# Kernel optimization log

Hardware: AMD Instinct MI355X
Metric: run time of the kernel (lower is better)

The kernel has to match this reference:

```python
import jax, jax.numpy as jnp
import numpy as np

V, E, H, B, T, S = 32000, 512, 512, 16, 128, 128


def setup_inputs() -> dict:
    key = jax.random.key(0)
    ks = jax.random.split(key, 12)
    sc_e = 1.0 / np.sqrt(E)
    sc_h = 1.0 / np.sqrt(H)
    emb_table = jax.random.normal(ks[0], (V, E), jnp.float32) * 0.02
    emb_table = emb_table.at[0].set(0.0)  # padding_idx=0
    return {
        "text_vec": jax.random.randint(ks[1], (B, T), 0, V),
        "decoder_hidden": jax.random.normal(ks[2], (1, B, H), jnp.float32),
        "encoder_output": jax.random.normal(ks[3], (B, S, H), jnp.float32),
        "attention_mask": jnp.ones((B, S), jnp.bool_),
        "emb_table": emb_table,
        "w_ih": jax.random.uniform(ks[4], (3 * H, E), jnp.float32, -sc_h, sc_h),
        "w_hh": jax.random.uniform(ks[5], (3 * H, H), jnp.float32, -sc_h, sc_h),
        "b_ih": jax.random.uniform(ks[6], (3 * H,), jnp.float32, -sc_h, sc_h),
        "b_hh": jax.random.uniform(ks[7], (3 * H,), jnp.float32, -sc_h, sc_h),
        "lin_out_w": jax.random.uniform(ks[8], (H, 2 * H), jnp.float32, -1.0 / np.sqrt(2 * H), 1.0 / np.sqrt(2 * H)),
        "out_w": jax.random.uniform(ks[9], (V, H), jnp.float32, -sc_h, sc_h),
        "out_b": jax.random.uniform(ks[10], (V,), jnp.float32, -sc_h, sc_h),
    }


def _gru_cell(x, h, w_ih, w_hh, b_ih, b_hh):
    gi = x @ w_ih.T + b_ih  # [B,3H]
    gh = h @ w_hh.T + b_hh  # [B,3H]
    ir, iz, inn = jnp.split(gi, 3, axis=-1)
    hr, hz, hn = jnp.split(gh, 3, axis=-1)
    r = jax.nn.sigmoid(ir + hr)
    z = jax.nn.sigmoid(iz + hz)
    n = jnp.tanh(inn + r * hn)
    return (1.0 - z) * n + z * h


def reference(text_vec, decoder_hidden, encoder_output, attention_mask,
              emb_table, w_ih, w_hh, b_ih, b_hh, lin_out_w, out_w, out_b):
    # embedding with padding_idx=0 -> zero vector
    emb = emb_table[text_vec] * (text_vec != 0)[..., None].astype(emb_table.dtype)  # [B,T,E]
    neg = jnp.asarray(-1e6, emb.dtype)

    def step(h, x_t):
        h_new = _gru_cell(x_t, h, w_ih, w_hh, b_ih, b_hh)  # [B,H]
        scores = jnp.einsum('bh,bsh->bs', h_new, encoder_output)
        scores = jnp.where(attention_mask, scores, neg)
        attn_w = jax.nn.softmax(scores, axis=-1)  # [B,S]
        mix = jnp.einsum('bs,bsh->bh', attn_w, encoder_output)
        combined = jnp.concatenate([h_new, mix], axis=-1)  # [B,2H]
        attended = jnp.tanh(combined @ lin_out_w.T)  # [B,H]
        return h_new, (attended, attn_w)

    h0 = decoder_hidden[0]  # num_layers == 1
    h_final, (attended_seq, attn_w_log) = jax.lax.scan(step, h0, jnp.swapaxes(emb, 0, 1))
    output = jnp.swapaxes(attended_seq, 0, 1)  # [B,T,H]
    scores = output @ out_w.T + out_b  # [B,T,V]
    return scores, h_final[None], attn_w_log
```

## Files before the change

### kernel.cpp

```cpp
#include <hip/hip_runtime.h>
#include <hip/hip_bf16.h>

#define NV 32000
#define NE 512
#define NH 512
#define NB 16
#define NT 128
#define NS 128

typedef __bf16 bf16x8 __attribute__((ext_vector_type(8)));
typedef float f32x4 __attribute__((ext_vector_type(4)));
typedef const __attribute__((address_space(1))) unsigned int gu32;
typedef __attribute__((address_space(3))) unsigned int lu32;

static constexpr size_t HTAG_OFF  = 0;
static constexpr size_t HDONE_OFF = HTAG_OFF + (size_t)2*NB*NH*8;
static constexpr size_t GI_OFF    = HDONE_OFF + 8192;
static constexpr size_t HALL_OFF  = GI_OFF + (size_t)NT*NB*3*NH*4;
static constexpr size_t MIX_OFF   = HALL_OFF + (size_t)(NT+1)*NB*NH*4;
static constexpr size_t ATTB_OFF  = MIX_OFF + (size_t)NB*NT*NH*4;
static constexpr size_t OWB_OFF   = ATTB_OFF + (size_t)NB*NT*NH*2;
static constexpr size_t WS_NEED   = OWB_OFF + (size_t)NV*NH*2;

__global__ __launch_bounds__(256) void k_pg(const int* __restrict__ tv,
                                            const float* __restrict__ emb,
                                            const float* __restrict__ w_ih,
                                            const float* __restrict__ b_ih,
                                            float* __restrict__ gi_all) {
  __shared__ float sbuf[2048];
  const int g = blockIdx.x;
  const int tid = threadIdx.x;
  float (*As)[64] = (float (*)[64])sbuf;
  float (*Bs)[64] = (float (*)[64])(sbuf + 1024);
  const int n0 = (g % 24) * 64;
  const int m0 = (g / 24) * 64;
  float acc[4][4] = {};
  const int rl = tid >> 2;
  const int kq = (tid & 3) * 4;
  const int tvr = tv[m0 + rl];
  const float* arow = emb + (long long)tvr * NE;
  const int tm = tid & 15, tn = tid >> 4;
  for (int k0 = 0; k0 < NE; k0 += 16) {
    __syncthreads();
    float4 av = make_float4(0.f, 0.f, 0.f, 0.f);
    if (tvr != 0) av = *(const float4*)(arow + k0 + kq);
    float4 bv = *(const float4*)(w_ih + (long long)(n0 + rl) * NE + k0 + kq);
    As[kq + 0][rl] = av.x; As[kq + 1][rl] = av.y; As[kq + 2][rl] = av.z; As[kq + 3][rl] = av.w;
    Bs[kq + 0][rl] = bv.x; Bs[kq + 1][rl] = bv.y; Bs[kq + 2][rl] = bv.z; Bs[kq + 3][rl] = bv.w;
    __syncthreads();
#pragma unroll
    for (int kk = 0; kk < 16; ++kk) {
      float4 a = *(const float4*)&As[kk][tm * 4];
      float4 b = *(const float4*)&Bs[kk][tn * 4];
      float ar[4] = {a.x, a.y, a.z, a.w}, br[4] = {b.x, b.y, b.z, b.w};
#pragma unroll
      for (int i = 0; i < 4; ++i)
#pragma unroll
        for (int j = 0; j < 4; ++j) acc[i][j] = fmaf(ar[i], br[j], acc[i][j]);
    }
  }
#pragma unroll
  for (int i = 0; i < 4; ++i) {
    int r = m0 + tm * 4 + i;
    long long gb = (long long)((r & 127) * 16 + (r >> 7)) * (3 * NH);
#pragma unroll
    for (int j = 0; j < 4; ++j) {
      int jg = n0 + tn * 4 + j;
      gi_all[gb + jg] = acc[i][j] + b_ih[jg];
    }
  }
}

__global__ __launch_bounds__(512, 1) void k_mid(const float* __restrict__ w_hh,
                                                const float* __restrict__ gi_all,
                                                const float* __restrict__ b_hh,
                                                const float* __restrict__ dh,
                                                float* __restrict__ h_all,
                                                unsigned long long* __restrict__ htag,
                                                unsigned int* __restrict__ hdone,
                                                float* __restrict__ d_hf,
                                                const float* __restrict__ enc,
                                                const int* __restrict__ mask,
                                                const float* __restrict__ out_w,
                                                __bf16* __restrict__ owb,
                                                float* __restrict__ d_attn,
                                                float* __restrict__ mixb) {
  __shared__ char smem_raw[86016];
  float* smem = (float*)smem_raw;
  const int tid = threadIdx.x;
  const int bid = blockIdx.x;

  if (bid < 128) {
    const int b = bid & 15, sub = bid >> 4;
    const int hl = tid & 63, kc = tid >> 6;
    const int j = sub * 64 + hl;
    float* hbuf = smem;
    float* part = smem + 512;

    float wg[3][64];
#pragma unroll
    for (int g = 0; g < 3; ++g) {
      const float* wp = w_hh + (long long)(g * 512 + j) * NH + kc * 64;
#pragma unroll
      for (int q4 = 0; q4 < 16; ++q4) {
        float4 w4 = *(const float4*)(wp + q4 * 4);
        wg[g][q4 * 4 + 0] = w4.x; wg[g][q4 * 4 + 1] = w4.y;
        wg[g][q4 * 4 + 2] = w4.z; wg[g][q4 * 4 + 3] = w4.w;
      }
    }
    float bhr = 0.f, bhz = 0.f, bhn = 0.f;
    if (tid < 64) {
      bhr = b_hh[sub * 64 + tid];
      bhz = b_hh[512 + sub * 64 + tid];
      bhn = b_hh[1024 + sub * 64 + tid];
    }

    for (int t = 0; t < NT; ++t) {
      float gr = 0.f, gz = 0.f, gn = 0.f;
      if (tid < 64) {
        const float* gi = gi_all + (long long)(t * 16 + b) * 1536;
        gr = gi[sub * 64 + tid];
        gz = gi[512 + sub * 64 + tid];
        gn = gi[1024 + sub * 64 + tid];
      }
      if (t == 0) {
        hbuf[tid] = dh[b * 512 + tid];
      } else {
        unsigned long long* slot = htag + ((long long)(t & 1) * NB + b) * 512 + tid;
        unsigned long long v = __hip_atomic_load(slot, __ATOMIC_RELAXED, __HIP_MEMORY_SCOPE_AGENT);
        int guard = 0;
        while ((unsigned)(v >> 32) != (unsigned)(t + 1) && ++guard < (1 << 22)) {
          v = __hip_atomic_load(slot, __ATOMIC_RELAXED, __HIP_MEMORY_SCOPE_AGENT);
        }
        union { unsigned u; float f; } c; c.u = (unsigned)v;
        hbuf[tid] = c.f;
      }
      __syncthreads();
      float ar = 0.f, az = 0.f, an = 0.f;
#pragma unroll
      for (int q4 = 0; q4 < 4; ++q4) {
        float4 h4[4];
#pragma unroll
        for (int u = 0; u < 4; ++u) h4[u] = *(const float4*)&hbuf[kc * 64 + q4 * 16 + u * 4];
#pragma unroll
        for (int u = 0; u < 4; ++u) {
          const float hh[4] = {h4[u].x, h4[u].y, h4[u].z, h4[u].w};
#pragma unroll
          for (int v = 0; v < 4; ++v) {
            const int q = q4 * 16 + u * 4 + v;
            ar = fmaf(hh[v], wg[0][q], ar);
            az = fmaf(hh[v], wg[1][q], az);
            an = fmaf(hh[v], wg[2][q], an);
          }
        }
      }
      part[(0 * 8 + kc) * 64 + hl] = ar;
      part[(1 * 8 + kc) * 64 + hl] = az;
      part[(2 * 8 + kc) * 64 + hl] = an;
      __syncthreads();
      if (tid < 64) {
        float sr = bhr, sz = bhz, sn = bhn;
#pragma unroll
        for (int c = 0; c < 8; ++c) {
          sr += part[(0 * 8 + c) * 64 + tid];
          sz += part[(1 * 8 + c) * 64 + tid];
          sn += part[(2 * 8 + c) * 64 + tid];
        }
        float r = 1.f / (1.f + expf(-(gr + sr)));
        float z = 1.f / (1.f + expf(-(gz + sz)));
        float n = tanhf(gn + r * sn);
        float hp = hbuf[sub * 64 + tid];
        float hv = (1.f - z) * n + z * hp;
        if (t < NT - 1) {
          union { float f; unsigned u; } c2; c2.f = hv;
          unsigned long long out = ((unsigned long long)(unsigned)(t + 2) << 32) | c2.u;
          __hip_atomic_store(htag + ((long long)((t + 1) & 1) * NB + b) * 512 + sub * 64 + tid, out,
                             __ATOMIC_RELAXED, __HIP_MEMORY_SCOPE_AGENT);
        }
        __hip_atomic_store(&h_all[(long long)((t + 1) * 16 + b) * 512 + sub * 64 + tid], hv,
                           __ATOMIC_RELAXED, __HIP_MEMORY_SCOPE_AGENT);
        if (t == NT - 1) d_hf[b * 512 + sub * 64 + tid] = hv;
      }
      __syncthreads();
      if (tid == 0)
        __hip_atomic_fetch_add(&hdone[t * 16 + b], 1u, __ATOMIC_RELAXED, __HIP_MEMORY_SCOPE_AGENT);
    }
    return;
  }

  const int cid = bid - 128;
  {
    long long n4 = (long long)NV * NH / 4;
    for (long long i = (long long)cid * 512 + tid; i < n4; i += (long long)128 * 512) {
      float4 v = ((const float4*)out_w)[i];
      union { __bf16 b[4]; float2 f2; } u;
      u.b[0] = (__bf16)v.x; u.b[1] = (__bf16)v.y; u.b[2] = (__bf16)v.z; u.b[3] = (__bf16)v.w;
      *((float2*)((__bf16*)owb + 4 * i)) = u.f2;
    }
  }
  float* hb = smem;
  float* red = smem + 512;
  float* wb = smem + 1024;
  float* sred = smem + 1152;
  for (int it = 0; it < 16; ++it) {
    const int u = it * 128 + cid;
    const int t = u >> 4, b = u & 15;
    if (tid == 0) {
      int guard = 0;
      while (__hip_atomic_load(&hdone[u], __ATOMIC_RELAXED, __HIP_MEMORY_SCOPE_AGENT) < 8u &&
             ++guard < (1 << 25)) {
        __builtin_amdgcn_s_sleep(4);
      }
    }
    __syncthreads();
    hb[tid] = __hip_atomic_load(&h_all[(long long)((t + 1) * 16 + b) * 512 + tid],
                                __ATOMIC_RELAXED, __HIP_MEMORY_SCOPE_AGENT);
    __syncthreads();
    {
      const int s = tid & 127, q = tid >> 7;
      const float* erow = enc + (long long)(b * 128 + s) * 512 + q * 128;
      float p = 0.f;
#pragma unroll 8
      for (int k = 0; k < 128; ++k) p = fmaf(hb[q * 128 + k], erow[k], p);
      red[tid] = p;
    }
    __syncthreads();
    float sc = 0.f;
    if (tid < 128) {
      sc = red[tid] + red[tid + 128] + red[tid + 256] + red[tid + 384];
      if (mask[b * 128 + tid] == 0) sc = -1e6f;
      wb[tid] = sc;
    }
    __syncthreads();
    if (tid < 64) {
      float m2 = fmaxf(wb[tid], wb[tid + 64]);
      for (int off = 32; off; off >>= 1) m2 = fmaxf(m2, __shfl_down(m2, off));
      if (tid == 0) sred[0] = m2;
    }
    __syncthreads();
    if (tid < 128) wb[tid] = expf(sc - sred[0]);
    __syncthreads();
    if (tid < 64) {
      float s2 = wb[tid] + wb[tid + 64];
      for (int off = 32; off; off >>= 1) s2 += __shfl_down(s2, off);
      if (tid == 0) sred[1] = s2;
    }
    __syncthreads();
    {
      float inv = 1.f / sred[1];
      if (tid < 128) {
        float w = wb[tid] * inv;
        wb[tid] = w;
        d_attn[(long long)u * 128 + tid] = w;
      }
    }
    __syncthreads();
    {
      float m = 0.f;
#pragma unroll 8
      for (int s2 = 0; s2 < 128; ++s2)
        m = fmaf(wb[s2], enc[(long long)(b * 128 + s2) * 512 + tid], m);
      mixb[(long long)(b * 128 + t) * 512 + tid] = m;
    }
    __syncthreads();
  }
}

__global__ __launch_bounds__(256) void k_att_lin(const float* __restrict__ h_all,
                                                 const float* __restrict__ mix,
                                                 const float* __restrict__ W,
                                                 __bf16* __restrict__ attout) {
  __shared__ float As[16][64];
  __shared__ float Bs[16][64];
  const int tid = threadIdx.x;
  const int n0 = blockIdx.x * 64;
  const int m0 = blockIdx.y * 64;
  float acc[4][4] = {};
  const int rl = tid >> 2;
  const int kq = (tid & 3) * 4;
  const int tm = tid & 15, tn = tid >> 4;
  const int r_a = m0 + rl;
  const int b_a = r_a >> 7, t_a = r_a & 127;
  const float* hrow = h_all + (long long)((t_a + 1) * 16 + b_a) * 512;
  const float* mrow = mix + (long long)r_a * 512;
  for (int k0 = 0; k0 < 1024; k0 += 16) {
    __syncthreads();
    float4 av = (k0 < 512) ? *(const float4*)(hrow + k0 + kq)
                           : *(const float4*)(mrow + (k0 - 512) + kq);
    float4 bv = *(const float4*)(W + (long long)(n0 + rl) * 1024 + k0 + kq);
    As[kq + 0][rl] = av.x; As[kq + 1][rl] = av.y; As[kq + 2][rl] = av.z; As[kq + 3][rl] = av.w;
    Bs[kq + 0][rl] = bv.x; Bs[kq + 1][rl] = bv.y; Bs[kq + 2][rl] = bv.z; Bs[kq + 3][rl] = bv.w;
    __syncthreads();
#pragma unroll
    for (int kk = 0; kk < 16; ++kk) {
      float4 a = *(const float4*)&As[kk][tm * 4];
      float4 b = *(const float4*)&Bs[kk][tn * 4];
      float ar[4] = {a.x, a.y, a.z, a.w}, br[4] = {b.x, b.y, b.z, b.w};
#pragma unroll
      for (int i = 0; i < 4; ++i)
#pragma unroll
        for (int j = 0; j < 4; ++j) acc[i][j] = fmaf(ar[i], br[j], acc[i][j]);
    }
  }
#pragma unroll
  for (int i = 0; i < 4; ++i) {
    int r = m0 + tm * 4 + i;
#pragma unroll
    for (int j = 0; j < 4; ++j) {
      int o = n0 + tn * 4 + j;
      attout[(long long)r * 512 + o] = (__bf16)tanhf(acc[i][j]);
    }
  }
}

__global__ __launch_bounds__(256) void k_out(const __bf16* __restrict__ Abf,
                                             const __bf16* __restrict__ Bbf,
                                             const float* __restrict__ bias,
                                             float* __restrict__ Cout) {
  __shared__ __bf16 Al[128 * 32];
  __shared__ __bf16 Bl[128 * 32];
  const int tid = threadIdx.x;
  const int lane = tid & 63;
  const int wave = tid >> 6;
  const int wm = wave >> 1, wn = wave & 1;
  const int swz = (blockIdx.x & 7) * 500 + (blockIdx.x >> 3);
  const int m0 = (swz & 15) * 128, n0 = (swz >> 4) * 128;
  f32x4 acc[4][4] = {};
  const int lrow = lane >> 2;
  const int lcol = (((lane & 3) ^ ((lane >> 3) & 3)) * 8);
  const int lm = lane & 15, lc = lane >> 4;
  const int sw = (lm >> 1) & 3;
  for (int ks = 0; ks < 16; ++ks) {
    const int k0 = ks * 32;
    __syncthreads();
#pragma unroll
    for (int i = 0; i < 2; ++i) {
      int chunk = wave * 2 + i;
      int r = chunk * 16 + lrow;
      const __bf16* ga = Abf + (long long)(m0 + r) * NH + k0 + lcol;
      const __bf16* gb = Bbf + (long long)(n0 + r) * NH + k0 + lcol;
      __builtin_amdgcn_global_load_lds((gu32*)ga, (lu32*)((char*)Al + chunk * 1024), 16, 0, 0);
      __builtin_amdgcn_global_load_lds((gu32*)gb, (lu32*)((char*)Bl + chunk * 1024), 16, 0, 0);
    }
    __syncthreads();
    bf16x8 af[4], bfr[4];
#pragma unroll
    for (int i = 0; i < 4; ++i)
      af[i] = *(const bf16x8*)&Al[(wm * 64 + i * 16 + lm) * 32 + ((lc ^ sw) * 8)];
#pragma unroll
    for (int j = 0; j < 4; ++j)
      bfr[j] = *(const bf16x8*)&Bl[(wn * 64 + j * 16 + lm) * 32 + ((lc ^ sw) * 8)];
#pragma unroll
    for (int i = 0; i < 4; ++i)
#pragma unroll
      for (int j = 0; j < 4; ++j)
        acc[i][j] = __builtin_amdgcn_mfma_f32_16x16x32_bf16(bfr[j], af[i], acc[i][j], 0, 0, 0);
  }
  float4 bv[4];
#pragma unroll
  for (int j = 0; j < 4; ++j)
    bv[j] = *(const float4*)&bias[n0 + wn * 64 + j * 16 + lc * 4];
#pragma unroll
  for (int i = 0; i < 4; ++i) {
    long long rbase = (long long)(m0 + wm * 64 + i * 16 + lm) * NV;
#pragma unroll
    for (int j = 0; j < 4; ++j) {
      int c = n0 + wn * 64 + j * 16 + lc * 4;
      float4 o;
      o.x = acc[i][j][0] + bv[j].x;
      o.y = acc[i][j][1] + bv[j].y;
      o.z = acc[i][j][2] + bv[j].z;
      o.w = acc[i][j][3] + bv[j].w;
      *(float4*)&Cout[rbase + c] = o;
    }
  }
}

extern "C" void kernel_launch(void* const* d_in, const int* in_sizes, int n_in,
                              void* d_out, int out_size, void* d_ws, size_t ws_size,
                              hipStream_t stream) {
  const int* tv = (const int*)d_in[0];
  const float* dh = (const float*)d_in[1];
  const float* enc = (const float*)d_in[2];
  const int* mask = (const int*)d_in[3];
  const float* emb = (const float*)d_in[4];
  const float* w_ih = (const float*)d_in[5];
  const float* w_hh = (const float*)d_in[6];
  const float* b_ih = (const float*)d_in[7];
  const float* b_hh = (const float*)d_in[8];
  const float* lin_w = (const float*)d_in[9];
  const float* out_w = (const float*)d_in[10];
  const float* out_b = (const float*)d_in[11];
  float* dout = (float*)d_out;
  char* ws = (char*)d_ws;
  if (ws_size < WS_NEED) return;

  unsigned long long* htag = (unsigned long long*)(ws + HTAG_OFF);
  unsigned int* hdone = (unsigned int*)(ws + HDONE_OFF);
  float* gi_all = (float*)(ws + GI_OFF);
  float* h_all = (float*)(ws + HALL_OFF);
  float* mixb = (float*)(ws + MIX_OFF);
  __bf16* attb = (__bf16*)(ws + ATTB_OFF);
  __bf16* owb = (__bf16*)(ws + OWB_OFF);

  float* d_scores = dout;
  float* d_hf = dout + (long long)NB * NT * NV;
  float* d_attn = d_hf + NB * NH;

  hipMemsetAsync(ws + HTAG_OFF, 0, HDONE_OFF + 8192 - HTAG_OFF, stream);
  k_pg<<<768, 256, 0, stream>>>(tv, emb, w_ih, b_ih, gi_all);
  k_mid<<<256, 512, 0, stream>>>(w_hh, gi_all, b_hh, dh, h_all, htag, hdone, d_hf,
                                 enc, mask, out_w, owb, d_attn, mixb);
  k_att_lin<<<dim3(8, 32), 256, 0, stream>>>(h_all, mixb, lin_w, attb);
  k_out<<<4000, 256, 0, stream>>>(attb, owb, out_b, d_scores);
}
```

Measured before the change: 496.6 us.

## Fuse input-gate GEMM into persistent recurrent kernel with per-chunk readiness flags

Removes the separate k_pg launch and computes the input-projection GEMM (embedding times w_ih) inside the worker blocks of k_mid, which publish per-(batch, half-sequence) completion counters. The recurrent blocks wait on these flags every 64 steps, so the first half of the sequence can start before the whole projection finishes. This overlaps the projection with the serial GRU chain and drops one kernel launch, at the cost of delaying the out_w bf16 conversion and attention work in those blocks. It also removes the XOR LDS swizzle in k_out, which may bring back LDS bank conflicts.

```diff
diff --git a/kernel.cpp b/kernel.cpp
--- a/kernel.cpp
+++ b/kernel.cpp
@@ -15,69 +15,26 @@
 
 static constexpr size_t HTAG_OFF  = 0;
 static constexpr size_t HDONE_OFF = HTAG_OFF + (size_t)2*NB*NH*8;
-static constexpr size_t GI_OFF    = HDONE_OFF + 8192;
+static constexpr size_t GIF_OFF   = HDONE_OFF + 8192;
+static constexpr size_t GI_OFF    = GIF_OFF + 4096;
 static constexpr size_t HALL_OFF  = GI_OFF + (size_t)NT*NB*3*NH*4;
 static constexpr size_t MIX_OFF   = HALL_OFF + (size_t)(NT+1)*NB*NH*4;
 static constexpr size_t ATTB_OFF  = MIX_OFF + (size_t)NB*NT*NH*4;
 static constexpr size_t OWB_OFF   = ATTB_OFF + (size_t)NB*NT*NH*2;
 static constexpr size_t WS_NEED   = OWB_OFF + (size_t)NV*NH*2;
 
-__global__ __launch_bounds__(256) void k_pg(const int* __restrict__ tv,
-                                            const float* __restrict__ emb,
-                                            const float* __restrict__ w_ih,
-                                            const float* __restrict__ b_ih,
-                                            float* __restrict__ gi_all) {
-  __shared__ float sbuf[2048];
-  const int g = blockIdx.x;
-  const int tid = threadIdx.x;
-  float (*As)[64] = (float (*)[64])sbuf;
-  float (*Bs)[64] = (float (*)[64])(sbuf + 1024);
-  const int n0 = (g % 24) * 64;
-  const int m0 = (g / 24) * 64;
-  float acc[4][4] = {};
-  const int rl = tid >> 2;
-  const int kq = (tid & 3) * 4;
-  const int tvr = tv[m0 + rl];
-  const float* arow = emb + (long long)tvr * NE;
-  const int tm = tid & 15, tn = tid >> 4;
-  for (int k0 = 0; k0 < NE; k0 += 16) {
-    __syncthreads();
-    float4 av = make_float4(0.f, 0.f, 0.f, 0.f);
-    if (tvr != 0) av = *(const float4*)(arow + k0 + kq);
-    float4 bv = *(const float4*)(w_ih + (long long)(n0 + rl) * NE + k0 + kq);
-    As[kq + 0][rl] = av.x; As[kq + 1][rl] = av.y; As[kq + 2][rl] = av.z; As[kq + 3][rl] = av.w;
-    Bs[kq + 0][rl] = bv.x; Bs[kq + 1][rl] = bv.y; Bs[kq + 2][rl] = bv.z; Bs[kq + 3][rl] = bv.w;
-    __syncthreads();
-#pragma unroll
-    for (int kk = 0; kk < 16; ++kk) {
-      float4 a = *(const float4*)&As[kk][tm * 4];
-      float4 b = *(const float4*)&Bs[kk][tn * 4];
-      float ar[4] = {a.x, a.y, a.z, a.w}, br[4] = {b.x, b.y, b.z, b.w};
-#pragma unroll
-      for (int i = 0; i < 4; ++i)
-#pragma unroll
-        for (int j = 0; j < 4; ++j) acc[i][j] = fmaf(ar[i], br[j], acc[i][j]);
-    }
-  }
-#pragma unroll
-  for (int i = 0; i < 4; ++i) {
-    int r = m0 + tm * 4 + i;
-    long long gb = (long long)((r & 127) * 16 + (r >> 7)) * (3 * NH);
-#pragma unroll
-    for (int j = 0; j < 4; ++j) {
-      int jg = n0 + tn * 4 + j;
-      gi_all[gb + jg] = acc[i][j] + b_ih[jg];
-    }
-  }
-}
-
 __global__ __launch_bounds__(512, 1) void k_mid(const float* __restrict__ w_hh,
-                                                const float* __restrict__ gi_all,
                                                 const float* __restrict__ b_hh,
                                                 const float* __restrict__ dh,
                                                 float* __restrict__ h_all,
                                                 unsigned long long* __restrict__ htag,
                                                 unsigned int* __restrict__ hdone,
+                                                unsigned int* __restrict__ giflag,
+                                                float* __restrict__ gi_all,
+                                                const int* __restrict__ tv,
+                                                const float* __restrict__ emb,
+                                                const float* __restrict__ w_ih,
+                                                const float* __restrict__ b_ih,
                                                 float* __restrict__ d_hf,
                                                 const float* __restrict__ enc,
                                                 const int* __restrict__ mask,
@@ -116,12 +73,22 @@
     }
 
     for (int t = 0; t < NT; ++t) {
+      if ((t & 63) == 0) {
+        if (tid == 0) {
+          unsigned int* gf = &giflag[b * 2 + (t >> 6)];
+          int guard = 0;
+          while (__hip_atomic_load(gf, __ATOMIC_RELAXED, __HIP_MEMORY_SCOPE_AGENT) < 24u &&
+                 ++guard < (1 << 25)) {}
+          (void)__hip_atomic_load(gf, __ATOMIC_ACQUIRE, __HIP_MEMORY_SCOPE_AGENT);
+        }
+        __syncthreads();
+      }
       float gr = 0.f, gz = 0.f, gn = 0.f;
       if (tid < 64) {
-        const float* gi = gi_all + (long long)(t * 16 + b) * 1536;
-        gr = gi[sub * 64 + tid];
-        gz = gi[512 + sub * 64 + tid];
-        gn = gi[1024 + sub * 64 + tid];
+        float* gi = gi_all + (long long)(t * 16 + b) * 1536;
+        gr = __hip_atomic_load(gi + sub * 64 + tid, __ATOMIC_RELAXED, __HIP_MEMORY_SCOPE_AGENT);
+        gz = __hip_atomic_load(gi + 512 + sub * 64 + tid, __ATOMIC_RELAXED, __HIP_MEMORY_SCOPE_AGENT);
+        gn = __hip_atomic_load(gi + 1024 + sub * 64 + tid, __ATOMIC_RELAXED, __HIP_MEMORY_SCOPE_AGENT);
       }
       if (t == 0) {
         hbuf[tid] = dh[b * 512 + tid];
@@ -189,6 +156,58 @@
   }
 
   const int cid = bid - 128;
+  {
+    float (*As)[64] = (float (*)[64])smem;
+    float (*Bs)[64] = (float (*)[64])(smem + 1024);
+    for (int p = 0; p < 6; ++p) {
+      const int tt = p * 128 + cid;
+      const int chunk = tt / 384;
+      const int rem = tt % 384;
+      const int b = rem / 24, nt = rem % 24;
+      const int n0 = nt * 64;
+      const int m0 = b * 128 + chunk * 64;
+      float acc[2][4] = {};
+      const int rl = tid >> 3;
+      const int kq2 = (tid & 7) * 2;
+      const int tvr = tv[m0 + rl];
+      const float* arow = emb + (long long)tvr * NE;
+      const int tm = tid & 31, tn = tid >> 5;
+      for (int k0 = 0; k0 < NE; k0 += 16) {
+        __syncthreads();
+        float2 av = make_float2(0.f, 0.f);
+        if (tvr != 0) av = *(const float2*)(arow + k0 + kq2);
+        float2 bv = *(const float2*)(w_ih + (long long)(n0 + rl) * NE + k0 + kq2);
+        As[kq2 + 0][rl] = av.x; As[kq2 + 1][rl] = av.y;
+        Bs[kq2 + 0][rl] = bv.x; Bs[kq2 + 1][rl] = bv.y;
+        __syncthreads();
+#pragma unroll
+        for (int kk = 0; kk < 16; ++kk) {
+          float a0 = As[kk][tm * 2], a1 = As[kk][tm * 2 + 1];
+          float4 b4 = *(const float4*)&Bs[kk][tn * 4];
+          const float br[4] = {b4.x, b4.y, b4.z, b4.w};
+#pragma unroll
+          for (int jj = 0; jj < 4; ++jj) {
+            acc[0][jj] = fmaf(a0, br[jj], acc[0][jj]);
+            acc[1][jj] = fmaf(a1, br[jj], acc[1][jj]);
+          }
+        }
+      }
+#pragma unroll
+      for (int i = 0; i < 2; ++i) {
+        int r = m0 + tm * 2 + i;
+        long long gb = (long long)((r & 127) * 16 + (r >> 7)) * (3 * NH);
+#pragma unroll
+        for (int jj = 0; jj < 4; ++jj) {
+          int jg = n0 + tn * 4 + jj;
+          __hip_atomic_store(&gi_all[gb + jg], acc[i][jj] + b_ih[jg],
+                             __ATOMIC_RELAXED, __HIP_MEMORY_SCOPE_AGENT);
+        }
+      }
+      __syncthreads();
+      if (tid == 0)
+        __hip_atomic_fetch_add(&giflag[b * 2 + chunk], 1u, __ATOMIC_RELEASE, __HIP_MEMORY_SCOPE_AGENT);
+    }
+  }
   {
     long long n4 = (long long)NV * NH / 4;
     for (long long i = (long long)cid * 512 + tid; i < n4; i += (long long)128 * 512) {
@@ -327,9 +346,8 @@
   const int m0 = (swz & 15) * 128, n0 = (swz >> 4) * 128;
   f32x4 acc[4][4] = {};
   const int lrow = lane >> 2;
-  const int lcol = (((lane & 3) ^ ((lane >> 3) & 3)) * 8);
+  const int lcol = (lane & 3) * 8;
   const int lm = lane & 15, lc = lane >> 4;
-  const int sw = (lm >> 1) & 3;
   for (int ks = 0; ks < 16; ++ks) {
     const int k0 = ks * 32;
     __syncthreads();
@@ -345,11 +363,9 @@
     __syncthreads();
     bf16x8 af[4], bfr[4];
 #pragma unroll
-    for (int i = 0; i < 4; ++i)
-      af[i] = *(const bf16x8*)&Al[(wm * 64 + i * 16 + lm) * 32 + ((lc ^ sw) * 8)];
-#pragma unroll
-    for (int j = 0; j < 4; ++j)
-      bfr[j] = *(const bf16x8*)&Bl[(wn * 64 + j * 16 + lm) * 32 + ((lc ^ sw) * 8)];
+    for (int i = 0; i < 4; ++i) af[i] = *(const bf16x8*)&Al[(wm * 64 + i * 16 + lm) * 32 + lc * 8];
+#pragma unroll
+    for (int j = 0; j < 4; ++j) bfr[j] = *(const bf16x8*)&Bl[(wn * 64 + j * 16 + lm) * 32 + lc * 8];
 #pragma unroll
     for (int i = 0; i < 4; ++i)
 #pragma unroll
@@ -397,6 +413,7 @@
 
   unsigned long long* htag = (unsigned long long*)(ws + HTAG_OFF);
   unsigned int* hdone = (unsigned int*)(ws + HDONE_OFF);
+  unsigned int* giflag = (unsigned int*)(ws + GIF_OFF);
   float* gi_all = (float*)(ws + GI_OFF);
   float* h_all = (float*)(ws + HALL_OFF);
   float* mixb = (float*)(ws + MIX_OFF);
@@ -407,9 +424,9 @@
   float* d_hf = dout + (long long)NB * NT * NV;
   float* d_attn = d_hf + NB * NH;
 
-  hipMemsetAsync(ws + HTAG_OFF, 0, HDONE_OFF + 8192 - HTAG_OFF, stream);
-  k_pg<<<768, 256, 0, stream>>>(tv, emb, w_ih, b_ih, gi_all);
-  k_mid<<<256, 512, 0, stream>>>(w_hh, gi_all, b_hh, dh, h_all, htag, hdone, d_hf,
+  hipMemsetAsync(ws + HTAG_OFF, 0, GI_OFF - HTAG_OFF, stream);
+  k_mid<<<256, 512, 0, stream>>>(w_hh, b_hh, dh, h_all, htag, hdone, giflag, gi_all,
+                                 tv, emb, w_ih, b_ih, d_hf,
                                  enc, mask, out_w, owb, d_attn, mixb);
   k_att_lin<<<dim3(8, 32), 256, 0, stream>>>(h_all, mixb, lin_w, attb);
   k_out<<<4000, 256, 0, stream>>>(attb, owb, out_b, d_scores);
```

After: 688.4 us. 38.6% more time.
